# Optimization experiments

Hardware: AMD Instinct MI355X
Metric: run time of the kernel (lower is better)

The kernel has to match this reference:

```python
import jax, jax.numpy as jnp
import numpy as np

N, D = 8192, 1024


def setup_inputs() -> dict:
    key = jax.random.key(0)
    k1, k2, k3 = jax.random.split(key, 3)
    f_1 = jax.random.normal(k1, (N, D), dtype=jnp.float32)
    f_2 = jax.random.normal(k2, (N, D), dtype=jnp.float32)
    f_3 = jax.random.normal(k3, (N, D), dtype=jnp.float32)
    return {"f_1": f_1, "f_2": f_2, "f_3": f_3, "batch": 3}


def _svdvals(x):
    # torch.svd computes full U, S, V; only singular values are consumed.
    return jnp.linalg.svd(x, compute_uv=False)


def reference(f_1, f_2, f_3, batch):
    if batch == 2:
        s_1 = _svdvals(f_1)
        if f_2.shape[0] == 0:
            return s_1[0] ** 2
        s_2 = _svdvals(f_2)
        return s_1.mean() + s_2.mean()
    elif batch == 3:
        s_1 = _svdvals(f_1)
        s_2 = _svdvals(f_2)
        s_3 = _svdvals(f_3)
        return s_1[0] ** 2 + 0.5 * (s_2[0] ** 2 + s_3[0] ** 2)
```

## Files before the change

kernel.cpp:

```cpp
#include <hip/hip_runtime.h>


#define DIM 1024
#define NROW 8192
#define MSZ (DIM*DIM)
#define NS 5
#define NZ4 443148

typedef __attribute__((ext_vector_type(8))) short short8;
typedef __attribute__((ext_vector_type(4))) float f32x4;

__device__ inline float bf2f(unsigned short u) {
    union { unsigned i; float f; } x; x.i = ((unsigned)u) << 16; return x.f;
}
__device__ inline unsigned short f2bf(float f) {
    union { float f; unsigned i; } x; x.f = f;
    unsigned r = x.i + 0x7FFFu + ((x.i >> 16) & 1u);
    return (unsigned short)(r >> 16);
}
__device__ inline void gload16(const void* g, void* l) {
    __builtin_amdgcn_global_load_lds(
        (const __attribute__((address_space(1))) unsigned int*)g,
        (__attribute__((address_space(3))) unsigned int*)l, 16, 0, 0);
}

__global__ __launch_bounds__(256)
void tconv_k(const float* __restrict__ f0, const float* __restrict__ f1,
             const float* __restrict__ f2, unsigned short* __restrict__ ft,
             float* __restrict__ zbase) {
    const int m = blockIdx.z;
    const int tid = threadIdx.x;
    if (m == 0) {
        int flat = blockIdx.x + 16 * blockIdx.y;
        size_t i = (size_t)flat * 217 + tid;
        if (tid < 217 && i < NZ4)
            ((float4*)zbase)[i] = make_float4(0.f, 0.f, 0.f, 0.f);
    }
    const float* f = (m == 0) ? f0 : (m == 1 ? f1 : f2);
    unsigned short* o = ft + (size_t)m * DIM * NROW;
    __shared__ float T[64][68];
    const int c0 = blockIdx.x * 64, r0 = blockIdx.y * 64;
    const int cx = (tid & 15) * 4, ry = tid >> 4;
#pragma unroll
    for (int i = 0; i < 4; ++i) {
        int r = ry + i * 16;
        float4 v = *(const float4*)&f[(size_t)(r0 + r) * DIM + c0 + cx];
        T[cx + 0][r] = v.x;
        T[cx + 1][r] = v.y;
        T[cx + 2][r] = v.z;
        T[cx + 3][r] = v.w;
    }
    __syncthreads();
#pragma unroll
    for (int i = 0; i < 4; ++i) {
        int c = ry + i * 16;
        float4 g = *(const float4*)&T[c][cx];
        ushort4 u;
        u.x = f2bf(g.x); u.y = f2bf(g.y); u.z = f2bf(g.z); u.w = f2bf(g.w);
        *(ushort4*)&o[(size_t)(c0 + c) * NROW + r0 + cx] = u;
    }
}

__global__ __launch_bounds__(256)
void syrk_sk(const unsigned short* __restrict__ src, float* __restrict__ Gp) {
    const int b = blockIdx.x;
    const int ky = b & 3;
    const int q = b >> 2;
    const int m = q / 36;
    const int tile = q - m * 36;
    int idx = tile, ti = 0;
    while (idx >= 8 - ti) { idx -= 8 - ti; ++ti; }
    const int tj = ti + idx;
    const int i0 = ti * 128, j0 = tj * 128;
    const unsigned short* S = src + (size_t)m * DIM * NROW;
    float* G = Gp + ((size_t)m * 36 + tile) * 16384;
    const int k0b = ky << 11;

    __shared__ unsigned short As[2 * 128 * 32];
    __shared__ unsigned short Bs[2 * 128 * 32];

    const int tid = threadIdx.x, w = tid >> 6, lane = tid & 63;
    const int wi = w >> 1, wj = w & 1;

    f32x4 acc[4][4];
#pragma unroll
    for (int a = 0; a < 4; ++a)
#pragma unroll
        for (int c = 0; c < 4; ++c) acc[a][c] = (f32x4){0.f, 0.f, 0.f, 0.f};

    const int lr = lane >> 2;
    const int ksw = (((lane & 3) ^ ((lane >> 4) & 3)) * 8);
    const int fr = lane & 15;
    const int slot = (((lane >> 4) ^ ((fr >> 2) & 3)) * 8);

    for (int k0 = k0b; k0 < k0b + 2048; k0 += 64) {
#pragma unroll
        for (int h = 0; h < 2; ++h)
#pragma unroll
            for (int p = 0; p < 2; ++p) {
                int rr = w * 32 + p * 16;
                gload16(S + (size_t)(i0 + rr + lr) * NROW + k0 + h * 32 + ksw,
                        &As[h * 4096 + rr * 32]);
                gload16(S + (size_t)(j0 + rr + lr) * NROW + k0 + h * 32 + ksw,
                        &Bs[h * 4096 + rr * 32]);
            }
        __syncthreads();
#pragma unroll
        for (int h = 0; h < 2; ++h) {
            short8 af[4], bfv[4];
#pragma unroll
            for (int a = 0; a < 4; ++a)
                af[a] = *(const short8*)&As[h * 4096 + (wi * 64 + a * 16 + fr) * 32 + slot];
#pragma unroll
            for (int c = 0; c < 4; ++c)
                bfv[c] = *(const short8*)&Bs[h * 4096 + (wj * 64 + c * 16 + fr) * 32 + slot];
#pragma unroll
            for (int a = 0; a < 4; ++a)
#pragma unroll
                for (int c = 0; c < 4; ++c)
                    acc[a][c] = __builtin_amdgcn_mfma_f32_16x16x32_bf16(
                        af[a], bfv[c], acc[a][c], 0, 0, 0);
        }
        __syncthreads();
    }

    const int qr = (lane >> 4) * 4, cn = lane & 15;
#pragma unroll
    for (int a = 0; a < 4; ++a)
#pragma unroll
        for (int c = 0; c < 4; ++c) {
            int cl = wj * 64 + c * 16 + cn;
#pragma unroll
            for (int reg = 0; reg < 4; ++reg) {
                int rl = wi * 64 + a * 16 + qr + reg;
                atomicAdd(&G[rl * 128 + cl], acc[a][c][reg]);
            }
        }
}

__global__ __launch_bounds__(256)
void convert_k(const float* __restrict__ Gp, float* __restrict__ trout,
               unsigned short* __restrict__ dst) {
    const int m = blockIdx.z;
    int idx = blockIdx.x, ti = 0;
    while (idx >= 8 - ti) { idx -= 8 - ti; ++ti; }
    const int tj = ti + idx;
    const int i0 = ti * 128, j0 = tj * 128;
    const float* G = Gp + ((size_t)m * 36 + blockIdx.x) * 16384;
    unsigned short* D = dst + (size_t)m * MSZ;
    __shared__ unsigned short T[128][136];
    const int tid = threadIdx.x;
    const int cx = (tid & 31) * 4, ry = tid >> 5;
    float dtr = 0.f;
#pragma unroll 4
    for (int t = 0; t < 16; ++t) {
        int r = ry + t * 8;
        float4 g = *(const float4*)&G[r * 128 + cx];
        ushort4 o;
        o.x = f2bf(g.x); o.y = f2bf(g.y); o.z = f2bf(g.z); o.w = f2bf(g.w);
        *(ushort4*)&D[(size_t)(i0 + r) * DIM + j0 + cx] = o;
        int rs = r ^ (cx & 124);
        T[cx + 0][rs] = o.x; T[cx + 1][rs] = o.y;
        T[cx + 2][rs] = o.z; T[cx + 3][rs] = o.w;
        if (ti == tj) {
            int d = r - cx;
            if (d >= 0 && d < 4)
                dtr += (d == 0 ? g.x : d == 1 ? g.y : d == 2 ? g.z : g.w);
        }
    }
    if (ti == tj) atomicAdd(&trout[m], dtr);
    if (ti != tj) {
        __syncthreads();
#pragma unroll 4
        for (int t = 0; t < 16; ++t) {
            int p = ry + t * 8;
            int qs = cx ^ (p & 124);
            ushort4 o = *(const ushort4*)&T[p][qs];
            *(ushort4*)&D[(size_t)(j0 + p) * DIM + i0 + cx] = o;
        }
    }
}

__global__ __launch_bounds__(256)
void sq_k(const unsigned short* __restrict__ src, const float* __restrict__ trin,
          float* __restrict__ trout, unsigned short* __restrict__ dst,
          float* __restrict__ vout) {
    const int m = blockIdx.z;
    const unsigned short* S = src + (size_t)m * MSZ;
    unsigned short* D = dst + (size_t)m * MSZ;
    int idx = blockIdx.x, ti = 0;
    while (idx >= 16 - ti) { idx -= 16 - ti; ++ti; }
    const int tj = ti + idx;
    const int i0 = ti * 64, j0 = tj * 64;
    float tv = trin[m];
    const float sc = 1.f / (tv * tv);

    __shared__ unsigned short As[2 * 64 * 32];
    __shared__ unsigned short Bs[2 * 64 * 32];
    __shared__ unsigned short Ts[64][68];
    __shared__ float rs[64], cs[64];

    const int tid = threadIdx.x, w = tid >> 6, lane = tid & 63;
    const int wi = w >> 1, wj = w & 1;
    f32x4 acc[2][2];
#pragma unroll
    for (int a = 0; a < 2; ++a)
#pragma unroll
        for (int b = 0; b < 2; ++b) acc[a][b] = (f32x4){0.f, 0.f, 0.f, 0.f};

    const int lr = lane >> 2;
    const int ksw = (((lane & 3) ^ ((lane >> 4) & 3)) * 8);
    const int fr = lane & 15;
    const int slot = (((lane >> 4) ^ ((fr >> 2) & 3)) * 8);

    for (int k0 = 0; k0 < DIM; k0 += 64) {
#pragma unroll
        for (int h = 0; h < 2; ++h) {
            gload16(S + (size_t)(i0 + w * 16 + lr) * DIM + k0 + h * 32 + ksw,
                    &As[h * 2048 + w * 16 * 32]);
            gload16(S + (size_t)(j0 + w * 16 + lr) * DIM + k0 + h * 32 + ksw,
                    &Bs[h * 2048 + w * 16 * 32]);
        }
        __syncthreads();
#pragma unroll
        for (int h = 0; h < 2; ++h) {
            short8 af[2], bfv[2];
#pragma unroll
            for (int a = 0; a < 2; ++a)
                af[a] = *(const short8*)&As[h * 2048 + (wi * 32 + a * 16 + fr) * 32 + slot];
#pragma unroll
            for (int c = 0; c < 2; ++c)
                bfv[c] = *(const short8*)&Bs[h * 2048 + (wj * 32 + c * 16 + fr) * 32 + slot];
#pragma unroll
            for (int a = 0; a < 2; ++a)
#pragma unroll
                for (int c = 0; c < 2; ++c)
                    acc[a][c] = __builtin_amdgcn_mfma_f32_16x16x32_bf16(
                        af[a], bfv[c], acc[a][c], 0, 0, 0);
        }
        __syncthreads();
    }

    if (vout) {
        if (tid < 64) rs[tid] = 0.f;
        else if (tid < 128) cs[tid - 64] = 0.f;
        __syncthreads();
    }

    const int qr = (lane >> 4) * 4, cn = lane & 15;
    float rsum[2][4] = {{0.f, 0.f, 0.f, 0.f}, {0.f, 0.f, 0.f, 0.f}};
    float csum[2] = {0.f, 0.f};
#pragma unroll
    for (int a = 0; a < 2; ++a)
#pragma unroll
        for (int b = 0; b < 2; ++b) {
            int cl = wj * 32 + b * 16 + cn;
#pragma unroll
            for (int reg = 0; reg < 4; ++reg) {
                int rl = wi * 32 + a * 16 + qr + reg;
                float vv = acc[a][b][reg] * sc;
                unsigned short val = f2bf(vv);
                D[(size_t)(i0 + rl) * DIM + j0 + cl] = val;
                Ts[cl][rl] = val;
                rsum[a][reg] += vv;
                csum[b] += vv;
            }
        }
    if (vout) {
#pragma unroll
        for (int a = 0; a < 2; ++a)
#pragma unroll
            for (int reg = 0; reg < 4; ++reg)
                atomicAdd(&rs[wi * 32 + a * 16 + qr + reg], rsum[a][reg]);
        if (ti != tj) {
#pragma unroll
            for (int b = 0; b < 2; ++b)
                atomicAdd(&cs[wj * 32 + b * 16 + cn], csum[b]);
        }
    }
    if (ti == tj && wi == wj) {
        int d = cn - qr;
        if (d >= 0 && d < 4)
            atomicAdd(&trout[m], (acc[0][0][d] + acc[1][1][d]) * sc);
    }
    if (ti != tj) {
        __syncthreads();
        const int cx = (tid & 15) * 4, ry = tid >> 4;
#pragma unroll
        for (int tq = 0; tq < 4; ++tq) {
            int p = ry + tq * 16;
            ushort4 o;
            o.x = Ts[p][cx + 0]; o.y = Ts[p][cx + 1];
            o.z = Ts[p][cx + 2]; o.w = Ts[p][cx + 3];
            *(ushort4*)&D[(size_t)(j0 + p) * DIM + i0 + cx] = o;
        }
    }
    if (vout) {
        __syncthreads();
        if (tid < 64) atomicAdd(&vout[m * DIM + i0 + tid], rs[tid]);
        else if (tid < 128 && ti != tj)
            atomicAdd(&vout[m * DIM + j0 + tid - 64], cs[tid - 64]);
    }
}

__global__ __launch_bounds__(256)
void mv_bf16(const unsigned short* __restrict__ M, const float* __restrict__ vin,
             float* __restrict__ vout, float* __restrict__ den) {
    int m = blockIdx.y;
    const unsigned short* A = M + (size_t)m * MSZ;
    int wv = threadIdx.x >> 6, lane = threadIdx.x & 63;
    int row = blockIdx.x * 4 + wv;
    const unsigned short* a = A + (size_t)row * DIM;
    const float* v = vin + m * DIM;
    float s = 0.f;
    for (int j = lane; j < DIM; j += 64) s += bf2f(a[j]) * v[j];
    for (int off = 32; off; off >>= 1) s += __shfl_down(s, off);
    __shared__ float part[4];
    if (lane == 0) { vout[m * DIM + row] = s; part[wv] = s * s; }
    __syncthreads();
    if (threadIdx.x == 0)
        atomicAdd(&den[m], part[0] + part[1] + part[2] + part[3]);
}

__global__ __launch_bounds__(256)
void rayfinal_k(const float* __restrict__ Gp, const float* __restrict__ wv,
                float* __restrict__ num, float* __restrict__ den,
                unsigned int* __restrict__ ctr, float* __restrict__ out) {
    const int m = blockIdx.y;
    int idx = blockIdx.x, ti = 0;
    while (idx >= 8 - ti) { idx -= 8 - ti; ++ti; }
    const int tj = ti + idx;
    const float* G = Gp + ((size_t)m * 36 + blockIdx.x) * 16384;
    const float* wi = wv + m * DIM + ti * 128;
    const float* wj = wv + m * DIM + tj * 128;
    const int tid = threadIdx.x;
    const int r = tid >> 1, c0 = (tid & 1) * 64;
    float inner = 0.f;
    const float4* g4 = (const float4*)&G[r * 128 + c0];
    const float4* w4 = (const float4*)&wj[c0];
#pragma unroll
    for (int t = 0; t < 16; ++t) {
        float4 g = g4[t], ww = w4[t];
        inner += g.x * ww.x + g.y * ww.y + g.z * ww.z + g.w * ww.w;
    }
    float s = wi[r] * inner;
    for (int off = 32; off; off >>= 1) s += __shfl_down(s, off);
    __shared__ float part[4];
    int lane = tid & 63, wx = tid >> 6;
    if (lane == 0) part[wx] = s;
    __syncthreads();
    if (tid == 0) {
        float tot = part[0] + part[1] + part[2] + part[3];
        if (ti != tj) tot *= 2.f;
        atomicAdd(&num[m], tot);
        __threadfence();
        unsigned int old = atomicAdd(ctr, 1u);
        if (old == 107u) {
            float n0 = atomicAdd(&num[0], 0.f), n1 = atomicAdd(&num[1], 0.f);
            float n2 = atomicAdd(&num[2], 0.f);
            float d0 = atomicAdd(&den[0], 0.f), d1 = atomicAdd(&den[1], 0.f);
            float d2 = atomicAdd(&den[2], 0.f);
            out[0] = n0 / d0 + 0.5f * (n1 / d1 + n2 / d2);
        }
    }
}

extern "C" void kernel_launch(void* const* d_in, const int* in_sizes, int n_in,
                              void* d_out, int out_size, void* d_ws, size_t ws_size,
                              hipStream_t stream) {
    const float* f0 = (const float*)d_in[0];
    const float* f1 = (const float*)d_in[1];
    const float* f2 = (const float*)d_in[2];

    char* base = (char*)d_ws;
    unsigned short* ft = (unsigned short*)base;
    unsigned short* Q  = (unsigned short*)base;
    unsigned short* P  = (unsigned short*)(base + 50331648);
    float* G32 = (float*)(base + 56623104);
    float* trbuf = G32 + 1769472;
    float* num = trbuf + 40;
    float* den = trbuf + 43;
    unsigned int* ctr = (unsigned int*)(trbuf + 46);
    float* v = trbuf + 48;
    float* w = v + 3 * DIM;

    dim3 gt(DIM / 64, NROW / 64, 3);
    tconv_k<<<gt, 256, 0, stream>>>(f0, f1, f2, ft, G32);

    syrk_sk<<<432, 256, 0, stream>>>(ft, G32);
    convert_k<<<dim3(36, 1, 3), 256, 0, stream>>>(G32, trbuf, P);

    unsigned short* cur = P;
    unsigned short* nxt = Q;
    for (int s = 0; s < NS; ++s) {
        sq_k<<<dim3(136, 1, 3), 256, 0, stream>>>(
            cur, trbuf + s * 3, trbuf + (s + 1) * 3, nxt,
            (s == NS - 1) ? v : nullptr);
        unsigned short* t2 = cur; cur = nxt; nxt = t2;
    }

    dim3 gm(DIM / 4, 3, 1);
    mv_bf16<<<gm, 256, 0, stream>>>(cur, v, w, den);

    rayfinal_k<<<dim3(36, 3, 1), 256, 0, stream>>>(G32, w, num, den, ctr,
                                                   (float*)d_out);
}
```

Before: 298.5 us.

## Fuse Gram conversion into split-K SYRK via last-block counter, specialize final squaring

Removes the separate convert_k launch. The last of the four split-K blocks per tile, detected by an atomic counter, now converts the fp32 Gram tile to bf16, mirrors it and accumulates the trace. Workspace zeroing moves from tconv_k to a hipMemsetAsync. The squaring kernel is split into a lean version and a final version that also computes the row-sum vector, so the vout branches disappear. This saves a launch and some branching, but adds a threadfence and counter serialization at the end of SYRK.

```diff
diff --git a/kernel.cpp b/kernel.cpp
--- a/kernel.cpp
+++ b/kernel.cpp
@@ -5,7 +5,6 @@
 #define NROW 8192
 #define MSZ (DIM*DIM)
 #define NS 5
-#define NZ4 443148
 
 typedef __attribute__((ext_vector_type(8))) short short8;
 typedef __attribute__((ext_vector_type(4))) float f32x4;
@@ -26,20 +25,13 @@
 
 __global__ __launch_bounds__(256)
 void tconv_k(const float* __restrict__ f0, const float* __restrict__ f1,
-             const float* __restrict__ f2, unsigned short* __restrict__ ft,
-             float* __restrict__ zbase) {
+             const float* __restrict__ f2, unsigned short* __restrict__ ft) {
     const int m = blockIdx.z;
-    const int tid = threadIdx.x;
-    if (m == 0) {
-        int flat = blockIdx.x + 16 * blockIdx.y;
-        size_t i = (size_t)flat * 217 + tid;
-        if (tid < 217 && i < NZ4)
-            ((float4*)zbase)[i] = make_float4(0.f, 0.f, 0.f, 0.f);
-    }
     const float* f = (m == 0) ? f0 : (m == 1 ? f1 : f2);
     unsigned short* o = ft + (size_t)m * DIM * NROW;
     __shared__ float T[64][68];
     const int c0 = blockIdx.x * 64, r0 = blockIdx.y * 64;
+    const int tid = threadIdx.x;
     const int cx = (tid & 15) * 4, ry = tid >> 4;
 #pragma unroll
     for (int i = 0; i < 4; ++i) {
@@ -62,7 +54,9 @@
 }
 
 __global__ __launch_bounds__(256)
-void syrk_sk(const unsigned short* __restrict__ src, float* __restrict__ Gp) {
+void syrk_sk(const unsigned short* __restrict__ src, float* __restrict__ Gp,
+             float* __restrict__ trout, unsigned int* __restrict__ tctr,
+             unsigned short* __restrict__ Pout) {
     const int b = blockIdx.x;
     const int ky = b & 3;
     const int q = b >> 2;
@@ -76,8 +70,10 @@
     float* G = Gp + ((size_t)m * 36 + tile) * 16384;
     const int k0b = ky << 11;
 
-    __shared__ unsigned short As[2 * 128 * 32];
-    __shared__ unsigned short Bs[2 * 128 * 32];
+    __shared__ __align__(16) unsigned char smem[34816];
+    unsigned short* As = (unsigned short*)smem;
+    unsigned short* Bs = As + 8192;
+    unsigned short* Tb = (unsigned short*)smem;
 
     const int tid = threadIdx.x, w = tid >> 6, lane = tid & 63;
     const int wi = w >> 1, wj = w & 1;
@@ -136,20 +132,16 @@
                 atomicAdd(&G[rl * 128 + cl], acc[a][c][reg]);
             }
         }
-}
-
-__global__ __launch_bounds__(256)
-void convert_k(const float* __restrict__ Gp, float* __restrict__ trout,
-               unsigned short* __restrict__ dst) {
-    const int m = blockIdx.z;
-    int idx = blockIdx.x, ti = 0;
-    while (idx >= 8 - ti) { idx -= 8 - ti; ++ti; }
-    const int tj = ti + idx;
-    const int i0 = ti * 128, j0 = tj * 128;
-    const float* G = Gp + ((size_t)m * 36 + blockIdx.x) * 16384;
-    unsigned short* D = dst + (size_t)m * MSZ;
-    __shared__ unsigned short T[128][136];
-    const int tid = threadIdx.x;
+
+    __threadfence();
+    __shared__ int lastf;
+    if (tid == 0)
+        lastf = (atomicAdd(&tctr[m * 36 + tile], 1u) == 3u);
+    __syncthreads();
+    if (!lastf) return;
+    __threadfence();
+
+    unsigned short* D = Pout + (size_t)m * MSZ;
     const int cx = (tid & 31) * 4, ry = tid >> 5;
     float dtr = 0.f;
 #pragma unroll 4
@@ -160,22 +152,25 @@
         o.x = f2bf(g.x); o.y = f2bf(g.y); o.z = f2bf(g.z); o.w = f2bf(g.w);
         *(ushort4*)&D[(size_t)(i0 + r) * DIM + j0 + cx] = o;
         int rs = r ^ (cx & 124);
-        T[cx + 0][rs] = o.x; T[cx + 1][rs] = o.y;
-        T[cx + 2][rs] = o.z; T[cx + 3][rs] = o.w;
+        Tb[(size_t)(cx + 0) * 136 + rs] = o.x;
+        Tb[(size_t)(cx + 1) * 136 + rs] = o.y;
+        Tb[(size_t)(cx + 2) * 136 + rs] = o.z;
+        Tb[(size_t)(cx + 3) * 136 + rs] = o.w;
         if (ti == tj) {
             int d = r - cx;
             if (d >= 0 && d < 4)
                 dtr += (d == 0 ? g.x : d == 1 ? g.y : d == 2 ? g.z : g.w);
         }
     }
-    if (ti == tj) atomicAdd(&trout[m], dtr);
-    if (ti != tj) {
+    if (ti == tj) {
+        atomicAdd(&trout[m], dtr);
+    } else {
         __syncthreads();
 #pragma unroll 4
         for (int t = 0; t < 16; ++t) {
             int p = ry + t * 8;
             int qs = cx ^ (p & 124);
-            ushort4 o = *(const ushort4*)&T[p][qs];
+            ushort4 o = *(const ushort4*)&Tb[(size_t)p * 136 + qs];
             *(ushort4*)&D[(size_t)(j0 + p) * DIM + i0 + cx] = o;
         }
     }
@@ -183,8 +178,7 @@
 
 __global__ __launch_bounds__(256)
 void sq_k(const unsigned short* __restrict__ src, const float* __restrict__ trin,
-          float* __restrict__ trout, unsigned short* __restrict__ dst,
-          float* __restrict__ vout) {
+          float* __restrict__ trout, unsigned short* __restrict__ dst) {
     const int m = blockIdx.z;
     const unsigned short* S = src + (size_t)m * MSZ;
     unsigned short* D = dst + (size_t)m * MSZ;
@@ -198,7 +192,6 @@
     __shared__ unsigned short As[2 * 64 * 32];
     __shared__ unsigned short Bs[2 * 64 * 32];
     __shared__ unsigned short Ts[64][68];
-    __shared__ float rs[64], cs[64];
 
     const int tid = threadIdx.x, w = tid >> 6, lane = tid & 63;
     const int wi = w >> 1, wj = w & 1;
@@ -241,11 +234,102 @@
         __syncthreads();
     }
 
-    if (vout) {
-        if (tid < 64) rs[tid] = 0.f;
-        else if (tid < 128) cs[tid - 64] = 0.f;
-        __syncthreads();
-    }
+    const int qr = (lane >> 4) * 4, cn = lane & 15;
+#pragma unroll
+    for (int a = 0; a < 2; ++a)
+#pragma unroll
+        for (int b = 0; b < 2; ++b) {
+            int cl = wj * 32 + b * 16 + cn;
+#pragma unroll
+            for (int reg = 0; reg < 4; ++reg) {
+                int rl = wi * 32 + a * 16 + qr + reg;
+                unsigned short val = f2bf(acc[a][b][reg] * sc);
+                D[(size_t)(i0 + rl) * DIM + j0 + cl] = val;
+                Ts[cl][rl] = val;
+            }
+        }
+    if (ti == tj && wi == wj) {
+        int d = cn - qr;
+        if (d >= 0 && d < 4)
+            atomicAdd(&trout[m], (acc[0][0][d] + acc[1][1][d]) * sc);
+    }
+    if (ti != tj) {
+        __syncthreads();
+        const int cx = (tid & 15) * 4, ry = tid >> 4;
+#pragma unroll
+        for (int tq = 0; tq < 4; ++tq) {
+            int p = ry + tq * 16;
+            ushort4 o;
+            o.x = Ts[p][cx + 0]; o.y = Ts[p][cx + 1];
+            o.z = Ts[p][cx + 2]; o.w = Ts[p][cx + 3];
+            *(ushort4*)&D[(size_t)(j0 + p) * DIM + i0 + cx] = o;
+        }
+    }
+}
+
+__global__ __launch_bounds__(256)
+void sq_last_k(const unsigned short* __restrict__ src, const float* __restrict__ trin,
+               float* __restrict__ trout, unsigned short* __restrict__ dst,
+               float* __restrict__ vout) {
+    const int m = blockIdx.z;
+    const unsigned short* S = src + (size_t)m * MSZ;
+    unsigned short* D = dst + (size_t)m * MSZ;
+    int idx = blockIdx.x, ti = 0;
+    while (idx >= 16 - ti) { idx -= 16 - ti; ++ti; }
+    const int tj = ti + idx;
+    const int i0 = ti * 64, j0 = tj * 64;
+    float tv = trin[m];
+    const float sc = 1.f / (tv * tv);
+
+    __shared__ unsigned short As[2 * 64 * 32];
+    __shared__ unsigned short Bs[2 * 64 * 32];
+    __shared__ unsigned short Ts[64][68];
+    __shared__ float rs[64], cs[64];
+
+    const int tid = threadIdx.x, w = tid >> 6, lane = tid & 63;
+    const int wi = w >> 1, wj = w & 1;
+    f32x4 acc[2][2];
+#pragma unroll
+    for (int a = 0; a < 2; ++a)
+#pragma unroll
+        for (int b = 0; b < 2; ++b) acc[a][b] = (f32x4){0.f, 0.f, 0.f, 0.f};
+
+    const int lr = lane >> 2;
+    const int ksw = (((lane & 3) ^ ((lane >> 4) & 3)) * 8);
+    const int fr = lane & 15;
+    const int slot = (((lane >> 4) ^ ((fr >> 2) & 3)) * 8);
+
+    for (int k0 = 0; k0 < DIM; k0 += 64) {
+#pragma unroll
+        for (int h = 0; h < 2; ++h) {
+            gload16(S + (size_t)(i0 + w * 16 + lr) * DIM + k0 + h * 32 + ksw,
+                    &As[h * 2048 + w * 16 * 32]);
+            gload16(S + (size_t)(j0 + w * 16 + lr) * DIM + k0 + h * 32 + ksw,
+                    &Bs[h * 2048 + w * 16 * 32]);
+        }
+        __syncthreads();
+#pragma unroll
+        for (int h = 0; h < 2; ++h) {
+            short8 af[2], bfv[2];
+#pragma unroll
+            for (int a = 0; a < 2; ++a)
+                af[a] = *(const short8*)&As[h * 2048 + (wi * 32 + a * 16 + fr) * 32 + slot];
+#pragma unroll
+            for (int c = 0; c < 2; ++c)
+                bfv[c] = *(const short8*)&Bs[h * 2048 + (wj * 32 + c * 16 + fr) * 32 + slot];
+#pragma unroll
+            for (int a = 0; a < 2; ++a)
+#pragma unroll
+                for (int c = 0; c < 2; ++c)
+                    acc[a][c] = __builtin_amdgcn_mfma_f32_16x16x32_bf16(
+                        af[a], bfv[c], acc[a][c], 0, 0, 0);
+        }
+        __syncthreads();
+    }
+
+    if (tid < 64) rs[tid] = 0.f;
+    else if (tid < 128) cs[tid - 64] = 0.f;
+    __syncthreads();
 
     const int qr = (lane >> 4) * 4, cn = lane & 15;
     float rsum[2][4] = {{0.f, 0.f, 0.f, 0.f}, {0.f, 0.f, 0.f, 0.f}};
@@ -266,17 +350,15 @@
                 csum[b] += vv;
             }
         }
-    if (vout) {
-#pragma unroll
-        for (int a = 0; a < 2; ++a)
-#pragma unroll
-            for (int reg = 0; reg < 4; ++reg)
-                atomicAdd(&rs[wi * 32 + a * 16 + qr + reg], rsum[a][reg]);
-        if (ti != tj) {
-#pragma unroll
-            for (int b = 0; b < 2; ++b)
-                atomicAdd(&cs[wj * 32 + b * 16 + cn], csum[b]);
-        }
+#pragma unroll
+    for (int a = 0; a < 2; ++a)
+#pragma unroll
+        for (int reg = 0; reg < 4; ++reg)
+            atomicAdd(&rs[wi * 32 + a * 16 + qr + reg], rsum[a][reg]);
+    if (ti != tj) {
+#pragma unroll
+        for (int b = 0; b < 2; ++b)
+            atomicAdd(&cs[wj * 32 + b * 16 + cn], csum[b]);
     }
     if (ti == tj && wi == wj) {
         int d = cn - qr;
@@ -295,12 +377,10 @@
             *(ushort4*)&D[(size_t)(j0 + p) * DIM + i0 + cx] = o;
         }
     }
-    if (vout) {
-        __syncthreads();
-        if (tid < 64) atomicAdd(&vout[m * DIM + i0 + tid], rs[tid]);
-        else if (tid < 128 && ti != tj)
-            atomicAdd(&vout[m * DIM + j0 + tid - 64], cs[tid - 64]);
-    }
+    __syncthreads();
+    if (tid < 64) atomicAdd(&vout[m * DIM + i0 + tid], rs[tid]);
+    else if (tid < 128 && ti != tj)
+        atomicAdd(&vout[m * DIM + j0 + tid - 64], cs[tid - 64]);
 }
 
 __global__ __launch_bounds__(256)
@@ -377,31 +457,36 @@
     unsigned short* Q  = (unsigned short*)base;
     unsigned short* P  = (unsigned short*)(base + 50331648);
     float* G32 = (float*)(base + 56623104);
-    float* trbuf = G32 + 1769472;
-    float* num = trbuf + 40;
-    float* den = trbuf + 43;
-    unsigned int* ctr = (unsigned int*)(trbuf + 46);
-    float* v = trbuf + 48;
+    float* scal = G32 + 1769472;
+    float* trbuf = scal;
+    float* num = scal + 24;
+    float* den = scal + 27;
+    unsigned int* fctr = (unsigned int*)(scal + 30);
+    unsigned int* tctr = (unsigned int*)(scal + 32);
+    float* v = scal + 160;
     float* w = v + 3 * DIM;
 
+    hipMemsetAsync(G32, 0, 7077888 + (160 + 3072) * 4, stream);
+
     dim3 gt(DIM / 64, NROW / 64, 3);
-    tconv_k<<<gt, 256, 0, stream>>>(f0, f1, f2, ft, G32);
-
-    syrk_sk<<<432, 256, 0, stream>>>(ft, G32);
-    convert_k<<<dim3(36, 1, 3), 256, 0, stream>>>(G32, trbuf, P);
+    tconv_k<<<gt, 256, 0, stream>>>(f0, f1, f2, ft);
+
+    syrk_sk<<<432, 256, 0, stream>>>(ft, G32, trbuf, tctr, P);
 
     unsigned short* cur = P;
     unsigned short* nxt = Q;
-    for (int s = 0; s < NS; ++s) {
-        sq_k<<<dim3(136, 1, 3), 256, 0, stream>>>(
-            cur, trbuf + s * 3, trbuf + (s + 1) * 3, nxt,
-            (s == NS - 1) ? v : nullptr);
+    for (int s = 0; s < NS - 1; ++s) {
+        sq_k<<<dim3(136, 1, 3), 256, 0, stream>>>(cur, trbuf + s * 3,
+                                                  trbuf + (s + 1) * 3, nxt);
         unsigned short* t2 = cur; cur = nxt; nxt = t2;
     }
+    sq_last_k<<<dim3(136, 1, 3), 256, 0, stream>>>(
+        cur, trbuf + (NS - 1) * 3, trbuf + NS * 3, nxt, v);
+    cur = nxt;
 
     dim3 gm(DIM / 4, 3, 1);
     mv_bf16<<<gm, 256, 0, stream>>>(cur, v, w, den);
 
-    rayfinal_k<<<dim3(36, 3, 1), 256, 0, stream>>>(G32, w, num, den, ctr,
+    rayfinal_k<<<dim3(36, 3, 1), 256, 0, stream>>>(G32, w, num, den, fctr,
                                                    (float*)d_out);
 }
```

Result: slower. 346.1 us (+16.0%).
